# Optimization experiments

Hardware: AMD Instinct MI355X
Metric: run time of the kernel (lower is better)

## Reference

```python
import math
import jax, jax.numpy as jnp
import numpy as np

SQRT_2_OVER_PI = 0.7978845608028654
EPS = 1e-5
EPS_VAR = 1e-4
NORM_EPS = 1e-12  # F.normalize default eps


def _gelu_tanh(x):
    return 0.5 * x * (1.0 + jnp.tanh(SQRT_2_OVER_PI * (x + 0.044715 * x ** 3)))


def _normalize(v, axis):
    n = jnp.linalg.norm(v, axis=axis, keepdims=True)
    return v / jnp.maximum(n, NORM_EPS)


def setup_inputs() -> dict:
    key = jax.random.key(0)
    k_x, k_m, k_o = jax.random.split(key, 3)
    B, T, D = 8, 2048, 512
    x = jax.random.normal(k_x, (B, T, D), dtype=jnp.float32)
    ema_mean = 0.1 * jax.random.normal(k_m, (D,), dtype=jnp.float32)
    ema_sq = ema_mean ** 2 + 1.0  # ensures positive variance, like a warmed-up EMA
    ema_out = jax.random.normal(k_o, (D,), dtype=jnp.float32)
    f32 = lambda v: jnp.asarray(v, dtype=jnp.float32)
    return {
        "x": x,
        "ema_mean": ema_mean,
        "ema_sq": ema_sq,
        "ema_out": ema_out,
        "log_tau": f32(math.log(2.0)),
        "log_beta_up": f32(math.log(math.exp(0.5) - 1.0)),
        "log_beta_dn": f32(math.log(math.exp(0.5) - 1.0)),
        "log_gamma": f32(math.log(math.exp(1.0) - 1.0)),
        "log_sigma_nn": f32(math.log(math.exp(1.0) - 1.0)),
        "log_w_nn": f32(math.log(math.exp(1.0) - 1.0)),
    }


def reference(x, ema_mean, ema_sq, ema_out, log_tau, log_beta_up,
              log_beta_dn, log_gamma, log_sigma_nn, log_w_nn):
    # Steady-state (_ready=True) forward path.
    sg = jax.lax.stop_gradient
    sp = jax.nn.softplus
    tau = jnp.exp(log_tau)
    beta_up, beta_dn = sp(log_beta_up), sp(log_beta_dn)
    gamma, sigma_nn, w_nn = sp(log_gamma), sp(log_sigma_nn), sp(log_w_nn)

    out = _gelu_tanh(x)  # [B,T,D]

    # --- per-channel asymmetric EMA z-score gate (z detached) ---
    var = jnp.clip(ema_sq - ema_mean ** 2, EPS_VAR, None)  # [D]
    std = jnp.sqrt(var)
    z = sg((x - ema_mean) / (std + EPS))  # [B,T,D]
    up_arm = beta_up * jax.nn.relu(jnp.tanh(gamma * z))
    dn_arm = beta_dn * jax.nn.relu(jnp.tanh(-gamma * z))
    gate_hist = jnp.clip(1.0 + up_arm - dn_arm, 0.05, 8.0)

    # --- within-sequence nearest-neighbor novelty gate (sim detached) ---
    T = x.shape[1]
    x_n = _normalize(sg(x), axis=-1)  # [B,T,D]
    sim = jnp.einsum('btd,bsd->bts', x_n, x_n)  # [B,T,T]
    sim = jnp.where(jnp.eye(T, dtype=bool)[None], -2.0, sim)
    nn_sim = jnp.max(sim, axis=-1)  # [B,T]
    novelty_nn = (1.0 - nn_sim) * 0.5
    surp_nn = sg(jnp.tanh(sigma_nn * novelty_nn))  # sigma_nn under no_grad
    gate_nn = (1.0 + w_nn * surp_nn)[..., None]  # [B,T,1]

    # --- cosine-to-EMA-output gate (fully detached, incl. tau) ---
    out_n = _normalize(out, axis=-1)
    ema_n = _normalize(ema_out, axis=0)  # [D]
    cos_sim = jnp.clip(jnp.sum(out_n * ema_n, axis=-1), -1.0, 1.0)  # [B,T]
    gate_cos = sg(jnp.exp(-tau * cos_sim))[..., None]  # [B,T,1]

    return out * gate_hist * gate_nn * gate_cos
```

## Files before the change

### kernel.cpp

```cpp
#include <hip/hip_runtime.h>
#include <hip/hip_bf16.h>
#include <math.h>

#define BB 8
#define TT 2048
#define DD 512
#define NSL 32

typedef __attribute__((ext_vector_type(8))) short bf16x8;
typedef __attribute__((ext_vector_type(4))) float f32x4;
typedef __attribute__((ext_vector_type(4))) int i32x4;

__device__ inline float softplus_f(float v) { return log1pf(expf(v)); }

__device__ inline float tanh_fast(float y) {
    float e = __builtin_amdgcn_exp2f(y * 2.8853900817779268f);
    return 1.0f - 2.0f * __builtin_amdgcn_rcpf(e + 1.0f);
}
__device__ inline float exp_fast(float y) {
    return __builtin_amdgcn_exp2f(y * 1.4426950408889634f);
}

__device__ inline unsigned short cvt_bf16(float f) {
    __hip_bfloat16 h = (__hip_bfloat16)f;
    return *reinterpret_cast<unsigned short*>(&h);
}
__device__ inline float bf2f(unsigned short h) {
    unsigned int u = ((unsigned int)h) << 16;
    return __uint_as_float(u);
}

__device__ inline void load_lds16(const void* g, void* l) {
    __builtin_amdgcn_global_load_lds(
        (const __attribute__((address_space(1))) unsigned int*)g,
        (__attribute__((address_space(3))) unsigned int*)l, 16, 0, 0);
}

__global__ __launch_bounds__(256) void k1_elem(
    const float* __restrict__ x, const float* __restrict__ ema_mean,
    const float* __restrict__ ema_sq, const float* __restrict__ ema_out,
    const float* __restrict__ p_log_tau, const float* __restrict__ p_lbu,
    const float* __restrict__ p_lbd, const float* __restrict__ p_lg,
    unsigned char* __restrict__ xn8, unsigned short* __restrict__ po) {
    const int row = blockIdx.x * 4 + (threadIdx.x >> 6);
    const int lane = threadIdx.x & 63;
    const size_t base = (size_t)row * DD;

    const float tau = expf(p_log_tau[0]);
    const float beta_up = softplus_f(p_lbu[0]);
    const float beta_dn = softplus_f(p_lbd[0]);
    const float gamma = softplus_f(p_lg[0]);

    float xv[8], pg[8];
    float sx2 = 0.f, so2 = 0.f, sod = 0.f, se2 = 0.f;
#pragma unroll
    for (int c = 0; c < 2; ++c) {
        const int j0 = c * 256 + lane * 4;
        float4 xx = *reinterpret_cast<const float4*>(x + base + j0);
        float4 mm = *reinterpret_cast<const float4*>(ema_mean + j0);
        float4 qq = *reinterpret_cast<const float4*>(ema_sq + j0);
        float4 eo = *reinterpret_cast<const float4*>(ema_out + j0);
        float vv[4] = {xx.x, xx.y, xx.z, xx.w};
        float vm[4] = {mm.x, mm.y, mm.z, mm.w};
        float vq[4] = {qq.x, qq.y, qq.z, qq.w};
        float ve[4] = {eo.x, eo.y, eo.z, eo.w};
#pragma unroll
        for (int q = 0; q < 4; ++q) {
            const int e = c * 4 + q;
            float xf = vv[q];
            xv[e] = xf;
            float x3 = xf * xf * xf;
            float gl = 0.5f * xf * (1.0f + tanh_fast(0.7978845608028654f * (xf + 0.044715f * x3)));
            float var = fmaxf(vq[q] - vm[q] * vm[q], 1e-4f);
            float istd = __builtin_amdgcn_rcpf(sqrtf(var) + 1e-5f);
            float z = (xf - vm[q]) * istd;
            float th = tanh_fast(gamma * z);
            float up = beta_up * fmaxf(th, 0.0f);
            float dn = beta_dn * fmaxf(-th, 0.0f);
            float gh = fminf(fmaxf(1.0f + up - dn, 0.05f), 8.0f);
            pg[e] = gl * gh;
            sx2 += xf * xf;
            so2 += gl * gl;
            sod += gl * ve[q];
            se2 += ve[q] * ve[q];
        }
    }
#pragma unroll
    for (int off = 32; off; off >>= 1) {
        sx2 += __shfl_xor(sx2, off);
        so2 += __shfl_xor(so2, off);
        sod += __shfl_xor(sod, off);
        se2 += __shfl_xor(se2, off);
    }
    const float qscale = 127.0f * __builtin_amdgcn_rcpf(fmaxf(sqrtf(sx2), 1e-12f));
    const float inv_en = __builtin_amdgcn_rcpf(fmaxf(sqrtf(se2), 1e-12f));
    float cosv = sod * inv_en * __builtin_amdgcn_rcpf(fmaxf(sqrtf(so2), 1e-12f));
    cosv = fminf(fmaxf(cosv, -1.0f), 1.0f);
    const float gcos = exp_fast(-tau * cosv);

#pragma unroll
    for (int c = 0; c < 2; ++c) {
        const int j0 = c * 256 + lane * 4;
        ushort4 pb;
        pb.x = cvt_bf16(pg[c * 4 + 0] * gcos);
        pb.y = cvt_bf16(pg[c * 4 + 1] * gcos);
        pb.z = cvt_bf16(pg[c * 4 + 2] * gcos);
        pb.w = cvt_bf16(pg[c * 4 + 3] * gcos);
        *reinterpret_cast<ushort4*>(po + base + j0) = pb;
        int q0 = __float2int_rn(xv[c * 4 + 0] * qscale);
        int q1 = __float2int_rn(xv[c * 4 + 1] * qscale);
        int q2 = __float2int_rn(xv[c * 4 + 2] * qscale);
        int q3 = __float2int_rn(xv[c * 4 + 3] * qscale);
        int pk = (q0 & 255) | ((q1 & 255) << 8) | ((q2 & 255) << 16) | (q3 << 24);
        *reinterpret_cast<int*>(xn8 + base + j0) = pk;
    }
}

__global__ __launch_bounds__(256, 4) void k2_nn(const unsigned char* __restrict__ xn8,
                                                float* __restrict__ partial) {
    __shared__ char lds[32768];

    const int tid = threadIdx.x;
    const int wave = tid >> 6;
    const int lane = tid & 63;
    const int r15 = lane & 15;
    const int kgrp = lane >> 4;
    const int wr = wave >> 1;
    const int wc = wave & 1;

    const int bid = blockIdx.x;
    const int b = bid & 7;
    int t = bid >> 3;
    int tm = 0;
    while (t >= 16 - tm) { t -= 16 - tm; ++tm; }
    const int tn = tm + t;

    const size_t bbase = (size_t)b * TT * DD;
    const unsigned char* Ag = xn8 + bbase + (size_t)tm * 128 * DD;
    const unsigned char* Bg = xn8 + bbase + (size_t)tn * 128 * DD;

    i32x4 acc[4][4];
#pragma unroll
    for (int i = 0; i < 4; ++i)
#pragma unroll
        for (int j = 0; j < 4; ++j) acc[i][j] = (i32x4){0, 0, 0, 0};

    auto stage = [&](int slot, int kt) {
#pragma unroll
        for (int l = 0; l < 2; ++l) {
            const int o = l * 4096 + tid * 16;
            const int sup = o >> 7;
            const int w = (o & 127) ^ ((sup & 7) << 4);
            const int row = sup * 2 + (w >> 6);
            const int cb = w & 63;
            load_lds16(Ag + (size_t)row * DD + kt * 64 + cb, lds + slot * 16384 + o);
            load_lds16(Bg + (size_t)row * DD + kt * 64 + cb, lds + slot * 16384 + 8192 + o);
        }
    };

#define LADDR(R) \
    (((R) >> 1) * 128 + (((((R) & 1) << 6) + (kgrp << 4)) ^ ((((R) >> 1) & 7) << 4)))

    auto compute = [&](int slot) {
        const char* sA = lds + slot * 16384;
        const char* sB = sA + 8192;
        i32x4 av[4], bv[4];
#pragma unroll
        for (int ni = 0; ni < 4; ++ni)
            bv[ni] = *(const i32x4*)(sB + LADDR(wc * 64 + ni * 16 + r15));
#pragma unroll
        for (int mi = 0; mi < 4; ++mi)
            av[mi] = *(const i32x4*)(sA + LADDR(wr * 64 + mi * 16 + r15));
        __builtin_amdgcn_s_setprio(1);
#pragma unroll
        for (int mi = 0; mi < 4; ++mi)
#pragma unroll
            for (int ni = 0; ni < 4; ++ni)
                acc[mi][ni] = __builtin_amdgcn_mfma_i32_16x16x64_i8(av[mi], bv[ni],
                                                                    acc[mi][ni], 0, 0, 0);
        __builtin_amdgcn_s_setprio(0);
    };
#undef LADDR

    stage(0, 0);
    __syncthreads();
#pragma unroll
    for (int kt = 0; kt < 8; ++kt) {
        if (kt < 7) stage((kt + 1) & 1, kt + 1);
        compute(kt & 1);
        if (kt < 7) __syncthreads();
    }

    const float inv_qq = 1.0f / (127.0f * 127.0f);
    const bool diag = (tm == tn);
    float accf[4][4][4];
#pragma unroll
    for (int mi = 0; mi < 4; ++mi)
#pragma unroll
        for (int ni = 0; ni < 4; ++ni)
#pragma unroll
            for (int rr = 0; rr < 4; ++rr) {
                float e = (float)acc[mi][ni][rr] * inv_qq;
                if (diag) {
                    const int rl = wr * 64 + mi * 16 + kgrp * 4 + rr;
                    const int cl = wc * 64 + ni * 16 + r15;
                    if (rl == cl) e = -2.0f;
                }
                accf[mi][ni][rr] = e;
            }
    float rmx[4][4];
#pragma unroll
    for (int mi = 0; mi < 4; ++mi)
#pragma unroll
        for (int rr = 0; rr < 4; ++rr) {
            float v = fmaxf(fmaxf(accf[mi][0][rr], accf[mi][1][rr]),
                            fmaxf(accf[mi][2][rr], accf[mi][3][rr]));
            v = fmaxf(v, __shfl_xor(v, 1));
            v = fmaxf(v, __shfl_xor(v, 2));
            v = fmaxf(v, __shfl_xor(v, 4));
            v = fmaxf(v, __shfl_xor(v, 8));
            rmx[mi][rr] = v;
        }
    float cmx[4];
#pragma unroll
    for (int ni = 0; ni < 4; ++ni) {
        float v = -2.0f;
#pragma unroll
        for (int mi = 0; mi < 4; ++mi)
#pragma unroll
            for (int rr = 0; rr < 4; ++rr) v = fmaxf(v, accf[mi][ni][rr]);
        v = fmaxf(v, __shfl_xor(v, 16));
        v = fmaxf(v, __shfl_xor(v, 32));
        cmx[ni] = v;
    }
    __syncthreads();
    float* rbuf = (float*)lds;
    float* cbuf = (float*)(lds + 1024);
    if (r15 == 0) {
#pragma unroll
        for (int mi = 0; mi < 4; ++mi)
#pragma unroll
            for (int rr = 0; rr < 4; ++rr)
                rbuf[(wr * 64 + mi * 16 + kgrp * 4 + rr) * 2 + wc] = rmx[mi][rr];
    }
    if (kgrp == 0) {
#pragma unroll
        for (int ni = 0; ni < 4; ++ni)
            cbuf[(wc * 64 + ni * 16 + r15) * 2 + wr] = cmx[ni];
    }
    __syncthreads();
    if (tid < 128) {
        const float v = fmaxf(rbuf[tid * 2 + 0], rbuf[tid * 2 + 1]);
        partial[((size_t)b * TT + tm * 128 + tid) * NSL + tn] = v;
    } else if (!diag) {
        const int c = tid - 128;
        const float v = fmaxf(cbuf[c * 2 + 0], cbuf[c * 2 + 1]);
        partial[((size_t)b * TT + tn * 128 + c) * NSL + 16 + tm] = v;
    }
}

__global__ __launch_bounds__(256) void k3_scale(float* __restrict__ out,
                                                const unsigned short* __restrict__ po,
                                                const float* __restrict__ partial,
                                                const float* __restrict__ p_lsn,
                                                const float* __restrict__ p_lwn) {
    const int row = blockIdx.x * 4 + (threadIdx.x >> 6);
    const int lane = threadIdx.x & 63;
    const float sigma_nn = softplus_f(p_lsn[0]);
    const float w_nn = softplus_f(p_lwn[0]);

    const int p = (row & (TT - 1)) >> 7;
    float v = -2.0f;
    if (lane < 16) {
        if (lane >= p) v = partial[(size_t)row * NSL + lane];
    } else if (lane < NSL) {
        if (lane - 16 < p) v = partial[(size_t)row * NSL + lane];
    }
    v = fmaxf(v, __shfl_xor(v, 1));
    v = fmaxf(v, __shfl_xor(v, 2));
    v = fmaxf(v, __shfl_xor(v, 4));
    v = fmaxf(v, __shfl_xor(v, 8));
    v = fmaxf(v, __shfl_xor(v, 16));
    v = fmaxf(v, __shfl_xor(v, 32));
    const float g = 1.0f + w_nn * tanh_fast(sigma_nn * 0.5f * (1.0f - v));

    const size_t base = (size_t)row * DD + lane * 8;
    ushort4 p0 = *reinterpret_cast<const ushort4*>(po + base);
    ushort4 p1 = *reinterpret_cast<const ushort4*>(po + base + 4);
    float4 o0, o1;
    o0.x = bf2f(p0.x) * g; o0.y = bf2f(p0.y) * g;
    o0.z = bf2f(p0.z) * g; o0.w = bf2f(p0.w) * g;
    o1.x = bf2f(p1.x) * g; o1.y = bf2f(p1.y) * g;
    o1.z = bf2f(p1.z) * g; o1.w = bf2f(p1.w) * g;
    *reinterpret_cast<float4*>(out + base) = o0;
    *reinterpret_cast<float4*>(out + base + 4) = o1;
}

extern "C" void kernel_launch(void* const* d_in, const int* in_sizes, int n_in,
                              void* d_out, int out_size, void* d_ws, size_t ws_size,
                              hipStream_t stream) {
    const float* x = (const float*)d_in[0];
    const float* ema_mean = (const float*)d_in[1];
    const float* ema_sq = (const float*)d_in[2];
    const float* ema_out = (const float*)d_in[3];
    const float* log_tau = (const float*)d_in[4];
    const float* log_beta_up = (const float*)d_in[5];
    const float* log_beta_dn = (const float*)d_in[6];
    const float* log_gamma = (const float*)d_in[7];
    const float* log_sigma_nn = (const float*)d_in[8];
    const float* log_w_nn = (const float*)d_in[9];

    char* ws = (char*)d_ws;
    unsigned char* XN8 = (unsigned char*)ws;
    unsigned short* PO = (unsigned short*)(ws + 8388608);
    float* partial = (float*)(ws + 8388608 + 16777216);
    float* out = (float*)d_out;

    hipLaunchKernelGGL(k1_elem, dim3(BB * TT / 4), dim3(256), 0, stream, x, ema_mean, ema_sq,
                       ema_out, log_tau, log_beta_up, log_beta_dn, log_gamma, XN8, PO);
    hipLaunchKernelGGL(k2_nn, dim3(BB * 136), dim3(256), 0, stream, XN8, partial);
    hipLaunchKernelGGL(k3_scale, dim3(BB * TT / 4), dim3(256), 0, stream, out, PO, partial,
                       log_sigma_nn, log_w_nn);
}
```

Measured before the change: 60.72 us.

## Triple-buffer LDS staging in NN similarity kernel and hoist loads in elementwise kernel

The int8 similarity GEMM kernel moves from double to triple buffering in LDS (48KB, occupancy hint lowered from 4 to 3 blocks/SM). It prefetches two k-tiles ahead and replaces __syncthreads with explicit vmcnt waits plus raw barriers so global-to-LDS loads overlap more compute. The elementwise kernel now issues all its global loads up front, before the scalar parameter math. The costs are lower occupancy and dependence on correct vmcnt counts, since the LDS writes are asynchronous.

```diff
diff --git a/kernel.cpp b/kernel.cpp
--- a/kernel.cpp
+++ b/kernel.cpp
@@ -45,6 +45,16 @@
     const int row = blockIdx.x * 4 + (threadIdx.x >> 6);
     const int lane = threadIdx.x & 63;
     const size_t base = (size_t)row * DD;
+    const int j0 = lane * 4, j1 = 256 + lane * 4;
+
+    float4 xx0 = *reinterpret_cast<const float4*>(x + base + j0);
+    float4 xx1 = *reinterpret_cast<const float4*>(x + base + j1);
+    float4 mm0 = *reinterpret_cast<const float4*>(ema_mean + j0);
+    float4 mm1 = *reinterpret_cast<const float4*>(ema_mean + j1);
+    float4 qq0 = *reinterpret_cast<const float4*>(ema_sq + j0);
+    float4 qq1 = *reinterpret_cast<const float4*>(ema_sq + j1);
+    float4 eo0 = *reinterpret_cast<const float4*>(ema_out + j0);
+    float4 eo1 = *reinterpret_cast<const float4*>(ema_out + j1);
 
     const float tau = expf(p_log_tau[0]);
     const float beta_up = softplus_f(p_lbu[0]);
@@ -53,37 +63,28 @@
 
     float xv[8], pg[8];
     float sx2 = 0.f, so2 = 0.f, sod = 0.f, se2 = 0.f;
-#pragma unroll
-    for (int c = 0; c < 2; ++c) {
-        const int j0 = c * 256 + lane * 4;
-        float4 xx = *reinterpret_cast<const float4*>(x + base + j0);
-        float4 mm = *reinterpret_cast<const float4*>(ema_mean + j0);
-        float4 qq = *reinterpret_cast<const float4*>(ema_sq + j0);
-        float4 eo = *reinterpret_cast<const float4*>(ema_out + j0);
-        float vv[4] = {xx.x, xx.y, xx.z, xx.w};
-        float vm[4] = {mm.x, mm.y, mm.z, mm.w};
-        float vq[4] = {qq.x, qq.y, qq.z, qq.w};
-        float ve[4] = {eo.x, eo.y, eo.z, eo.w};
-#pragma unroll
-        for (int q = 0; q < 4; ++q) {
-            const int e = c * 4 + q;
-            float xf = vv[q];
-            xv[e] = xf;
-            float x3 = xf * xf * xf;
-            float gl = 0.5f * xf * (1.0f + tanh_fast(0.7978845608028654f * (xf + 0.044715f * x3)));
-            float var = fmaxf(vq[q] - vm[q] * vm[q], 1e-4f);
-            float istd = __builtin_amdgcn_rcpf(sqrtf(var) + 1e-5f);
-            float z = (xf - vm[q]) * istd;
-            float th = tanh_fast(gamma * z);
-            float up = beta_up * fmaxf(th, 0.0f);
-            float dn = beta_dn * fmaxf(-th, 0.0f);
-            float gh = fminf(fmaxf(1.0f + up - dn, 0.05f), 8.0f);
-            pg[e] = gl * gh;
-            sx2 += xf * xf;
-            so2 += gl * gl;
-            sod += gl * ve[q];
-            se2 += ve[q] * ve[q];
-        }
+    float vv[8] = {xx0.x, xx0.y, xx0.z, xx0.w, xx1.x, xx1.y, xx1.z, xx1.w};
+    float vm[8] = {mm0.x, mm0.y, mm0.z, mm0.w, mm1.x, mm1.y, mm1.z, mm1.w};
+    float vq[8] = {qq0.x, qq0.y, qq0.z, qq0.w, qq1.x, qq1.y, qq1.z, qq1.w};
+    float ve[8] = {eo0.x, eo0.y, eo0.z, eo0.w, eo1.x, eo1.y, eo1.z, eo1.w};
+#pragma unroll
+    for (int e = 0; e < 8; ++e) {
+        float xf = vv[e];
+        xv[e] = xf;
+        float x3 = xf * xf * xf;
+        float gl = 0.5f * xf * (1.0f + tanh_fast(0.7978845608028654f * (xf + 0.044715f * x3)));
+        float var = fmaxf(vq[e] - vm[e] * vm[e], 1e-4f);
+        float istd = __builtin_amdgcn_rcpf(sqrtf(var) + 1e-5f);
+        float z = (xf - vm[e]) * istd;
+        float th = tanh_fast(gamma * z);
+        float up = beta_up * fmaxf(th, 0.0f);
+        float dn = beta_dn * fmaxf(-th, 0.0f);
+        float gh = fminf(fmaxf(1.0f + up - dn, 0.05f), 8.0f);
+        pg[e] = gl * gh;
+        sx2 += xf * xf;
+        so2 += gl * gl;
+        sod += gl * ve[e];
+        se2 += ve[e] * ve[e];
     }
 #pragma unroll
     for (int off = 32; off; off >>= 1) {
@@ -100,25 +101,25 @@
 
 #pragma unroll
     for (int c = 0; c < 2; ++c) {
-        const int j0 = c * 256 + lane * 4;
+        const int j = c * 256 + lane * 4;
         ushort4 pb;
         pb.x = cvt_bf16(pg[c * 4 + 0] * gcos);
         pb.y = cvt_bf16(pg[c * 4 + 1] * gcos);
         pb.z = cvt_bf16(pg[c * 4 + 2] * gcos);
         pb.w = cvt_bf16(pg[c * 4 + 3] * gcos);
-        *reinterpret_cast<ushort4*>(po + base + j0) = pb;
+        *reinterpret_cast<ushort4*>(po + base + j) = pb;
         int q0 = __float2int_rn(xv[c * 4 + 0] * qscale);
         int q1 = __float2int_rn(xv[c * 4 + 1] * qscale);
         int q2 = __float2int_rn(xv[c * 4 + 2] * qscale);
         int q3 = __float2int_rn(xv[c * 4 + 3] * qscale);
         int pk = (q0 & 255) | ((q1 & 255) << 8) | ((q2 & 255) << 16) | (q3 << 24);
-        *reinterpret_cast<int*>(xn8 + base + j0) = pk;
-    }
-}
-
-__global__ __launch_bounds__(256, 4) void k2_nn(const unsigned char* __restrict__ xn8,
+        *reinterpret_cast<int*>(xn8 + base + j) = pk;
+    }
+}
+
+__global__ __launch_bounds__(256, 3) void k2_nn(const unsigned char* __restrict__ xn8,
                                                 float* __restrict__ partial) {
-    __shared__ char lds[32768];
+    __shared__ char lds[49152];
 
     const int tid = threadIdx.x;
     const int wave = tid >> 6;
@@ -183,12 +184,23 @@
 #undef LADDR
 
     stage(0, 0);
-    __syncthreads();
+    stage(1, 1);
+    asm volatile("s_waitcnt vmcnt(4)" ::: "memory");
+    __builtin_amdgcn_s_barrier();
+    __builtin_amdgcn_sched_barrier(0);
+
 #pragma unroll
     for (int kt = 0; kt < 8; ++kt) {
-        if (kt < 7) stage((kt + 1) & 1, kt + 1);
-        compute(kt & 1);
-        if (kt < 7) __syncthreads();
+        if (kt + 2 < 8) stage((kt + 2) % 3, kt + 2);
+        compute(kt % 3);
+        if (kt < 7) {
+            if (kt + 2 < 8)
+                asm volatile("s_waitcnt vmcnt(4)" ::: "memory");
+            else
+                asm volatile("s_waitcnt vmcnt(0)" ::: "memory");
+            __builtin_amdgcn_s_barrier();
+            __builtin_amdgcn_sched_barrier(0);
+        }
     }
 
     const float inv_qq = 1.0f / (127.0f * 127.0f);
```

After: 60.01 us. Within noise of the previous version (-1.2%).
